# Kernel tuning notes

Measured on AMD Instinct MI355X. Metric: run time of the kernel, lower is better.

The kernel has to match this reference:

```python
import jax, jax.numpy as jnp
import numpy as np


def _grid_sample_bilinear_border(img, grid):
    """Faithful jax port of F.grid_sample(mode='bilinear', padding_mode='border',
    align_corners=False). img: [B,C,H,W], grid: [B,Hg,Wg,2] (x,y in [-1,1]).
    Returns [B,C,Hg,Wg]."""
    B, C, H, W = img.shape
    gx, gy = grid[..., 0], grid[..., 1]           # [B,Hg,Wg]
    # unnormalize (align_corners=False)
    ix = ((gx + 1.0) * W - 1.0) * 0.5
    iy = ((gy + 1.0) * H - 1.0) * 0.5
    ix0f = jnp.floor(ix)
    iy0f = jnp.floor(iy)
    wx = (ix - ix0f)[:, None]                     # [B,1,Hg,Wg] broadcast over C
    wy = (iy - iy0f)[:, None]
    x0 = jnp.clip(ix0f.astype(jnp.int32), 0, W - 1)
    x1 = jnp.clip(ix0f.astype(jnp.int32) + 1, 0, W - 1)
    y0 = jnp.clip(iy0f.astype(jnp.int32), 0, H - 1)
    y1 = jnp.clip(iy0f.astype(jnp.int32) + 1, 0, H - 1)

    def gather(im, yy, xx):                       # im [C,H,W], yy/xx [Hg,Wg]
        return im[:, yy, xx]                      # [C,Hg,Wg]

    g = jax.vmap(gather)
    v00 = g(img, y0, x0)
    v01 = g(img, y0, x1)
    v10 = g(img, y1, x0)
    v11 = g(img, y1, x1)
    return (v00 * (1.0 - wx) * (1.0 - wy)
            + v01 * wx * (1.0 - wy)
            + v10 * (1.0 - wx) * wy
            + v11 * wx * wy)


def setup_inputs() -> dict:
    key = jax.random.key(0)
    k1, k2, k3 = jax.random.split(key, 3)
    B, C, V, D, P = 1, 16, 360, 736, 16384        # batch, ch, views, detectors, recon pixels
    sinogram = jax.random.normal(k1, (B, C, V, D), dtype=jnp.float32)
    grid = jax.random.uniform(k2, (B, V, P, 2), dtype=jnp.float32,
                              minval=-1.1, maxval=1.1)
    square_inv = jax.random.uniform(k3, (B, 1, V, P), dtype=jnp.float32,
                                    minval=0.5, maxval=1.5) * 1e-3
    return {"sinogram": sinogram, "grid": grid, "square_inv": square_inv}


def reference(sinogram, grid, square_inv):
    # back_projection: bilinear gather over sinogram at grid coords, weight by
    # inverse-square distance, sum over the view axis (dim -2).
    sampled = _grid_sample_bilinear_border(sinogram, grid)   # [B,C,view,P]
    recon_img = jnp.sum(sampled * square_inv * 1000.0, axis=-2)  # [B,C,P]
    return recon_img
```

## Files before the change

kernel.cpp:

```cpp
#include <hip/hip_runtime.h>
#include <hip/hip_bf16.h>

#define NP 16384
#define NV 360
#define ND 736
#define NC 16
#define VSPLIT 32

__global__ __launch_bounds__(256) void sino_transpose_bf16(const float* __restrict__ sino,
                                                           ushort* __restrict__ st) {
    int idx = blockIdx.x * 256 + threadIdx.x;
    if (idx >= NV * ND) return;
    uint packed[8];
#pragma unroll
    for (int q = 0; q < 8; ++q) {
        uint ul = __float_as_uint(sino[(2 * q)     * (NV * ND) + idx]);
        uint uh = __float_as_uint(sino[(2 * q + 1) * (NV * ND) + idx]);
        ul = (ul + 0x7fffu + ((ul >> 16) & 1u)) >> 16;
        uh = (uh + 0x7fffu + ((uh >> 16) & 1u)) >> 16;
        packed[q] = ul | (uh << 16);
    }
    uint4* dst = reinterpret_cast<uint4*>(st + ((size_t)idx << 4));
    dst[0] = make_uint4(packed[0], packed[1], packed[2], packed[3]);
    dst[1] = make_uint4(packed[4], packed[5], packed[6], packed[7]);
}

__global__ __launch_bounds__(256) void backproj(const float* __restrict__ grd,
                                                const float* __restrict__ sq,
                                                const ushort* __restrict__ st,
                                                float* __restrict__ out) {
    int tid = blockIdx.x * 256 + threadIdx.x;
    int p  = tid & (NP - 1);
    int vs = tid >> 14;
    int v0 = (vs * NV) / VSPLIT;
    int v1 = ((vs + 1) * NV) / VSPLIT;

    float acc[NC];
#pragma unroll
    for (int c = 0; c < NC; ++c) acc[c] = 0.0f;

    const float2* grd2 = reinterpret_cast<const float2*>(grd);

    auto gather = [&](int idx, float w) {
        const uint4* pp = reinterpret_cast<const uint4*>(st + ((size_t)idx << 4));
        uint4 a = pp[0], b = pp[1];
        uint u[8] = {a.x, a.y, a.z, a.w, b.x, b.y, b.z, b.w};
#pragma unroll
        for (int q = 0; q < 8; ++q) {
            acc[2 * q]     = fmaf(__uint_as_float(u[q] << 16),         w, acc[2 * q]);
            acc[2 * q + 1] = fmaf(__uint_as_float(u[q] & 0xffff0000u), w, acc[2 * q + 1]);
        }
    };

    for (int v = v0; v < v1; ++v) {
        int gi = v * NP + p;
        float2 g = grd2[gi];
        float w  = sq[gi] * 1000.0f;

        float ix = ((g.x + 1.0f) * (float)ND - 1.0f) * 0.5f;
        float iy = ((g.y + 1.0f) * (float)NV - 1.0f) * 0.5f;
        float x0f = floorf(ix), y0f = floorf(iy);
        float wx = ix - x0f,   wy = iy - y0f;
        int x0i = (int)x0f, y0i = (int)y0f;
        int x0 = min(max(x0i,     0), ND - 1);
        int x1 = min(max(x0i + 1, 0), ND - 1);
        int y0 = min(max(y0i,     0), NV - 1);
        int y1 = min(max(y0i + 1, 0), NV - 1);

        float w00 = (1.0f - wx) * (1.0f - wy) * w;
        float w01 = wx * (1.0f - wy) * w;
        float w10 = (1.0f - wx) * wy * w;
        float w11 = wx * wy * w;

        gather(y0 * ND + x0, w00);
        gather(y0 * ND + x1, w01);
        gather(y1 * ND + x0, w10);
        gather(y1 * ND + x1, w11);
    }

#pragma unroll
    for (int c = 0; c < NC; ++c)
        atomicAdd(&out[c * NP + p], acc[c]);
}

extern "C" void kernel_launch(void* const* d_in, const int* in_sizes, int n_in,
                              void* d_out, int out_size, void* d_ws, size_t ws_size,
                              hipStream_t stream) {
    const float* sino = (const float*)d_in[0];
    const float* grd  = (const float*)d_in[1];
    const float* sq   = (const float*)d_in[2];
    float* out = (float*)d_out;
    ushort* st = (ushort*)d_ws;

    hipMemsetAsync(out, 0, (size_t)out_size * sizeof(float), stream);

    {
        int n = NV * ND;
        sino_transpose_bf16<<<(n + 255) / 256, 256, 0, stream>>>(sino, st);
    }
    {
        int nthreads = NP * VSPLIT;
        backproj<<<nthreads / 256, 256, 0, stream>>>(grd, sq, st, out);
    }
}
```

Baseline: 273.8 us.

## Split bf16 sinogram table into two 8-channel halves processed by separate blocks

The transposed bf16 sinogram goes from one 32-byte record per texel to two separate 16-byte planes, each holding 8 channels. Each backprojection block now handles one channel half, so a thread keeps 8 accumulators and does one 16-byte gather per corner instead of two. The grid doubles and paired blocks sit next to each other, which halves register pressure and the per-gather footprint. The cost is that the grid coordinates, weights and bilinear math are recomputed twice, and two accumulators are unrolled.

```diff
diff --git a/kernel.cpp b/kernel.cpp
--- a/kernel.cpp
+++ b/kernel.cpp
@@ -6,6 +6,7 @@
 #define ND 736
 #define NC 16
 #define VSPLIT 32
+#define QSZ (NV * ND * 8)
 
 __global__ __launch_bounds__(256) void sino_transpose_bf16(const float* __restrict__ sino,
                                                            ushort* __restrict__ st) {
@@ -20,38 +21,43 @@
         uh = (uh + 0x7fffu + ((uh >> 16) & 1u)) >> 16;
         packed[q] = ul | (uh << 16);
     }
-    uint4* dst = reinterpret_cast<uint4*>(st + ((size_t)idx << 4));
-    dst[0] = make_uint4(packed[0], packed[1], packed[2], packed[3]);
-    dst[1] = make_uint4(packed[4], packed[5], packed[6], packed[7]);
+    uint4* d0 = reinterpret_cast<uint4*>(st + ((size_t)idx << 3));
+    uint4* d1 = reinterpret_cast<uint4*>(st + QSZ + ((size_t)idx << 3));
+    *d0 = make_uint4(packed[0], packed[1], packed[2], packed[3]);
+    *d1 = make_uint4(packed[4], packed[5], packed[6], packed[7]);
 }
 
 __global__ __launch_bounds__(256) void backproj(const float* __restrict__ grd,
                                                 const float* __restrict__ sq,
                                                 const ushort* __restrict__ st,
                                                 float* __restrict__ out) {
-    int tid = blockIdx.x * 256 + threadIdx.x;
-    int p  = tid & (NP - 1);
-    int vs = tid >> 14;
+    int Q    = blockIdx.x & 1;
+    int r    = blockIdx.x >> 1;
+    int pblk = r & 63;
+    int vs   = r >> 6;
+    int p  = pblk * 256 + threadIdx.x;
     int v0 = (vs * NV) / VSPLIT;
     int v1 = ((vs + 1) * NV) / VSPLIT;
 
-    float acc[NC];
+    const ushort* __restrict__ tbl = st + Q * QSZ;
+
+    float acc[8];
 #pragma unroll
-    for (int c = 0; c < NC; ++c) acc[c] = 0.0f;
+    for (int c = 0; c < 8; ++c) acc[c] = 0.0f;
 
     const float2* grd2 = reinterpret_cast<const float2*>(grd);
 
     auto gather = [&](int idx, float w) {
-        const uint4* pp = reinterpret_cast<const uint4*>(st + ((size_t)idx << 4));
-        uint4 a = pp[0], b = pp[1];
-        uint u[8] = {a.x, a.y, a.z, a.w, b.x, b.y, b.z, b.w};
+        uint4 a = *reinterpret_cast<const uint4*>(tbl + ((size_t)idx << 3));
+        uint u[4] = {a.x, a.y, a.z, a.w};
 #pragma unroll
-        for (int q = 0; q < 8; ++q) {
+        for (int q = 0; q < 4; ++q) {
             acc[2 * q]     = fmaf(__uint_as_float(u[q] << 16),         w, acc[2 * q]);
             acc[2 * q + 1] = fmaf(__uint_as_float(u[q] & 0xffff0000u), w, acc[2 * q + 1]);
         }
     };
 
+#pragma unroll 2
     for (int v = v0; v < v1; ++v) {
         int gi = v * NP + p;
         float2 g = grd2[gi];
@@ -79,8 +85,8 @@
     }
 
 #pragma unroll
-    for (int c = 0; c < NC; ++c)
-        atomicAdd(&out[c * NP + p], acc[c]);
+    for (int c = 0; c < 8; ++c)
+        atomicAdd(&out[(Q * 8 + c) * NP + p], acc[c]);
 }
 
 extern "C" void kernel_launch(void* const* d_in, const int* in_sizes, int n_in,
@@ -99,7 +105,7 @@
         sino_transpose_bf16<<<(n + 255) / 256, 256, 0, stream>>>(sino, st);
     }
     {
-        int nthreads = NP * VSPLIT;
-        backproj<<<nthreads / 256, 256, 0, stream>>>(grd, sq, st, out);
+        int nblocks = 2 * 64 * VSPLIT;
+        backproj<<<nblocks, 256, 0, stream>>>(grd, sq, st, out);
     }
 }
```

Measured after the change: 290.1 us. 5.9% more time.
